# Kernel optimization log

Hardware: AMD Instinct MI355X
Metric: run time of the kernel (lower is better)

## Reference

```python
import jax, jax.numpy as jnp
import numpy as np

H, C, HID, L, NF, B = 4, 128, 128, 3, 5, 32  # heads, per-head dim, hidden, layers, node feats, graphs
LN_EPS = 1e-5


def setup_inputs() -> dict:
    key = jax.random.key(0)
    ks = jax.random.split(key, 12)
    N, E = 10000, 160000
    x = jax.random.normal(ks[0], (N, NF), dtype=jnp.float32)
    edge_index = jax.random.randint(ks[1], (2, E), 0, N, dtype=jnp.int64)
    batch = jnp.sort(jax.random.randint(ks[2], (N,), 0, B, dtype=jnp.int64))
    s = 0.1
    return {
        "x": x,
        "edge_index": edge_index,
        "batch": batch,
        "node_W": jax.random.normal(ks[3], (NF, HID), dtype=jnp.float32) * s,
        "node_b": jnp.zeros((HID,), dtype=jnp.float32),
        "Ws": jax.random.normal(ks[4], (L, HID, H * C), dtype=jnp.float32) * s,
        "att_srcs": jax.random.normal(ks[5], (L, H, C), dtype=jnp.float32) * s,
        "att_dsts": jax.random.normal(ks[6], (L, H, C), dtype=jnp.float32) * s,
        "biases": jnp.zeros((L, HID), dtype=jnp.float32),
        "ln_gs": jnp.ones((L, HID), dtype=jnp.float32),
        "ln_bs": jnp.zeros((L, HID), dtype=jnp.float32),
    }


def _layer_norm(x, g, b):
    mu = jnp.mean(x, axis=-1, keepdims=True)
    var = jnp.mean(jnp.square(x - mu), axis=-1, keepdims=True)
    return (x - mu) * jax.lax.rsqrt(var + LN_EPS) * g + b


def _gat_layer(x, W, att_src, att_dst, bias, src, dst, N):
    # x: [N, HID]; PyG GATConv, heads=H, concat=False (mean over heads)
    h = (x @ W).reshape(N, H, C)                       # [N,H,C]
    a_src = jnp.sum(h * att_src, axis=-1)              # [N,H]
    a_dst = jnp.sum(h * att_dst, axis=-1)              # [N,H]
    e = jax.nn.leaky_relu(a_src[src] + a_dst[dst], 0.2)  # [E,H]
    # edge-softmax over destination neighborhoods (numerically stable)
    m = jax.ops.segment_max(e, dst, num_segments=N)
    ex = jnp.exp(e - m[dst])
    denom = jax.ops.segment_sum(ex, dst, num_segments=N)
    alpha = ex / (denom[dst] + 1e-16)                  # [E,H]
    msg = h[src] * alpha[:, :, None]                   # [E,H,C]
    out = jax.ops.segment_sum(msg, dst, num_segments=N)  # [N,H,C]
    return out.mean(axis=1) + bias                     # concat=False -> head mean


def reference(x, edge_index, batch, node_W, node_b, Ws, att_srcs, att_dsts,
              biases, ln_gs, ln_bs):
    N = x.shape[0]
    loop = jnp.arange(N, dtype=edge_index.dtype)
    src = jnp.concatenate([edge_index[0], loop])       # PyG adds self-loops
    dst = jnp.concatenate([edge_index[1], loop])

    h = jax.nn.relu(x @ node_W + node_b)               # [N,HID]
    for l in range(L):
        h_new = _gat_layer(h, Ws[l], att_srcs[l], att_dsts[l], biases[l], src, dst, N)
        h_new = _layer_norm(h_new, ln_gs[l], ln_bs[l])
        h = jax.nn.relu(h_new) + h                     # residual; dropout is identity in eval

    # global mean pool over graphs
    sums = jax.ops.segment_sum(h, batch, num_segments=B)
    cnts = jax.ops.segment_sum(jnp.ones((N, 1), h.dtype), batch, num_segments=B)
    graph_emb = sums / jnp.maximum(cnts, 1.0)
    return h, graph_emb
```

## Files before the change

### kernel.cpp

```cpp
#include <hip/hip_runtime.h>
#include <math.h>

#define N_NODES 10000
#define N_EDGES 160000
#define E2 (N_EDGES + N_NODES)
#define HIDDEN 128
#define NHEAD 4
#define NB 32
#define LN_EPS 1e-5f

#define T_INPUT (N_NODES * HIDDEN)
#define T_HIST  (T_INPUT + N_EDGES)
#define T_CONV  (T_HIST + 3 * 512 * 128)
#define T_BOUND (T_CONV + N_NODES)
#define T_TOTAL T_BOUND

typedef __attribute__((ext_vector_type(8))) short bf16x8;
typedef __attribute__((ext_vector_type(4))) float f32x4;

__device__ __forceinline__ unsigned short f2bf(float f) {
    unsigned int u = __float_as_uint(f);
    u += 0x7fffu + ((u >> 16) & 1u);
    return (unsigned short)(u >> 16);
}
__device__ __forceinline__ float bf2f_lo(unsigned int u) { return __uint_as_float(u << 16); }
__device__ __forceinline__ float bf2f_hi(unsigned int u) { return __uint_as_float(u & 0xffff0000u); }

__global__ __launch_bounds__(256) void k_pre(const float* __restrict__ x,
                                             const float* __restrict__ W,
                                             const float* __restrict__ b,
                                             const int* __restrict__ ei,
                                             const int* __restrict__ batch,
                                             const float* __restrict__ Ws,
                                             float* __restrict__ h,
                                             unsigned short* __restrict__ hb,
                                             int* counts, int* gstart, int* gend,
                                             unsigned short* __restrict__ Btb) {
    int t = blockIdx.x * blockDim.x + threadIdx.x;
    if (t < T_INPUT) {
        int n = t >> 7, c = t & 127;
        float s = b[c];
        #pragma unroll
        for (int k = 0; k < 5; k++) s += x[n * 5 + k] * W[k * HIDDEN + c];
        float r = fmaxf(s, 0.f);
        h[t] = r;
        hb[t] = f2bf(r);
    } else if (t < T_HIST) {
        int e = t - T_INPUT;
        atomicAdd(&counts[ei[N_EDGES + e]], 1);
    } else if (t < T_CONV) {
        int i = t - T_HIST;
        int l = i >> 16, rem = i & 65535;
        int n = rem >> 7, k = rem & 127;
        Btb[i] = f2bf(Ws[l * 65536 + k * 512 + n]);
    } else if (t < T_BOUND) {
        int n = t - T_CONV;
        int bb = batch[n];
        if (n == 0 || batch[n - 1] != bb) gstart[bb] = n;
        if (n == N_NODES - 1 || batch[n + 1] != bb) gend[bb] = n + 1;
    }
}

__global__ void k_scan(const int* __restrict__ counts, int* rowptr, int* cursor) {
    __shared__ int sums[1024];
    int t = threadIdx.x;
    const int per = 10;
    int base = t * per;
    int loc[per];
    int s = 0;
    for (int i = 0; i < per; i++) {
        int idx = base + i;
        int v = (idx < N_NODES) ? counts[idx] + 1 : 0;
        loc[i] = s; s += v;
    }
    sums[t] = s;
    __syncthreads();
    for (int off = 1; off < 1024; off <<= 1) {
        int v = (t >= off) ? sums[t - off] : 0;
        __syncthreads();
        sums[t] += v;
        __syncthreads();
    }
    int prefix = (t > 0) ? sums[t - 1] : 0;
    for (int i = 0; i < per; i++) {
        int idx = base + i;
        if (idx < N_NODES) { int r = prefix + loc[i]; rowptr[idx] = r; cursor[idx] = r; }
    }
    if (t == 1023) rowptr[N_NODES] = sums[1023];
}

__global__ void k_scatter(const int* __restrict__ ei, int* cursor, int* csr_src) {
    int e = blockIdx.x * blockDim.x + threadIdx.x;
    if (e < N_EDGES) {
        int s = ei[e], d = ei[N_EDGES + e];
        int pos = atomicAdd(&cursor[d], 1);
        csr_src[pos] = s;
    } else if (e < E2) {
        int n = e - N_EDGES;
        int pos = atomicAdd(&cursor[n], 1);
        csr_src[pos] = n;
    }
}

__global__ __launch_bounds__(256) void k_gemm_att(const unsigned short* __restrict__ Ab,
                                                  const unsigned short* __restrict__ Bt,
                                                  const float* __restrict__ ws,
                                                  const float* __restrict__ wd,
                                                  unsigned short* __restrict__ Cb,
                                                  float* __restrict__ a_src,
                                                  float* __restrict__ a_dst) {
    int wave = threadIdx.x >> 6, lane = threadIdx.x & 63;
    int q = lane >> 4, u = lane & 15;
    int h = blockIdx.x;
    int rowgrp = wave & 1, colhalf = wave >> 1;
    int mbase = blockIdx.y * 32 + rowgrp * 16;
    int colbase = h * 128 + colhalf * 64;
    int arow = mbase + u;
    if (arow > N_NODES - 1) arow = N_NODES - 1;
    bf16x8 a[4];
    #pragma unroll
    for (int k0 = 0; k0 < 4; k0++)
        a[k0] = *(const bf16x8*)(Ab + (size_t)arow * 128 + k0 * 32 + q * 8);
    f32x4 acc[4];
    #pragma unroll
    for (int nb = 0; nb < 4; nb++) acc[nb] = (f32x4){0.f, 0.f, 0.f, 0.f};
    #pragma unroll
    for (int nb = 0; nb < 4; nb++) {
        const unsigned short* bp = Bt + (size_t)(colbase + nb * 16 + u) * 128 + q * 8;
        #pragma unroll
        for (int k0 = 0; k0 < 4; k0++) {
            bf16x8 bfr = *(const bf16x8*)(bp + k0 * 32);
            acc[nb] = __builtin_amdgcn_mfma_f32_16x16x32_bf16(a[k0], bfr, acc[nb], 0, 0, 0);
        }
    }
    #pragma unroll
    for (int nb = 0; nb < 4; nb++) {
        int col = colbase + nb * 16 + u;
        #pragma unroll
        for (int r = 0; r < 4; r++) {
            int row = mbase + q * 4 + r;
            if (row < N_NODES) Cb[(size_t)row * 512 + col] = f2bf(acc[nb][r]);
        }
    }
    float ps[4] = {}, pd[4] = {};
    #pragma unroll
    for (int nb = 0; nb < 4; nb++) {
        int cl = colhalf * 64 + nb * 16 + u;
        float wsv = ws[h * 128 + cl], wdv = wd[h * 128 + cl];
        #pragma unroll
        for (int r = 0; r < 4; r++) { ps[r] += acc[nb][r] * wsv; pd[r] += acc[nb][r] * wdv; }
    }
    #pragma unroll
    for (int d = 1; d < 16; d <<= 1) {
        #pragma unroll
        for (int r = 0; r < 4; r++) {
            ps[r] += __shfl_xor(ps[r], d);
            pd[r] += __shfl_xor(pd[r], d);
        }
    }
    __shared__ float ls[2][2][16], ldd[2][2][16];
    if (u == 0) {
        #pragma unroll
        for (int r = 0; r < 4; r++) {
            ls[rowgrp][colhalf][q * 4 + r] = ps[r];
            ldd[rowgrp][colhalf][q * 4 + r] = pd[r];
        }
    }
    __syncthreads();
    if (colhalf == 0 && lane < 16) {
        int row = mbase + lane;
        if (row < N_NODES) {
            a_src[row * 4 + h] = ls[rowgrp][0][lane] + ls[rowgrp][1][lane];
            a_dst[row * 4 + h] = ldd[rowgrp][0][lane] + ldd[rowgrp][1][lane];
        }
    }
}

__global__ __launch_bounds__(256) void k_agg(const uint4* __restrict__ hb4,
                                             const int* __restrict__ rowptr,
                                             const int* __restrict__ csr,
                                             const float* __restrict__ a_src,
                                             const float* __restrict__ a_dst,
                                             const float* __restrict__ bias,
                                             const float* __restrict__ lng,
                                             const float* __restrict__ lnb,
                                             float* __restrict__ h,
                                             unsigned short* __restrict__ hbn) {
    int wave = threadIdx.x >> 6;
    int lane = threadIdx.x & 63;
    int n = blockIdx.x * 4 + wave;
    if (n >= N_NODES) return;
    int hl = lane >> 4;
    int pos = lane & 15;
    int off = rowptr[n];
    int deg = rowptr[n + 1] - off;
    float adn = a_dst[n * 4 + hl];
    float m = -INFINITY, denom = 0.f;
    float o[8] = {};
    for (int base = 0; base < deg; base += 64) {
        int cnt = min(64, deg - base);
        int s = (lane < cnt) ? csr[off + base + lane] : 0;
        int si = __shfl(s, 0);
        uint4 u = hb4[(size_t)si * 64 + lane];
        float av = a_src[si * 4 + hl];
        for (int i = 0; i < cnt; i++) {
            int inext = (i + 1 < cnt) ? i + 1 : i;
            int sj = __shfl(s, inext);
            uint4 un = hb4[(size_t)sj * 64 + lane];
            float an = a_src[sj * 4 + hl];
            float t = av + adn;
            float e = t > 0.f ? t : 0.2f * t;
            float nm = fmaxf(m, e);
            float sc = __expf(m - nm);
            float p = __expf(e - nm);
            denom = denom * sc + p;
            o[0] = o[0] * sc + p * bf2f_lo(u.x);
            o[1] = o[1] * sc + p * bf2f_hi(u.x);
            o[2] = o[2] * sc + p * bf2f_lo(u.y);
            o[3] = o[3] * sc + p * bf2f_hi(u.y);
            o[4] = o[4] * sc + p * bf2f_lo(u.z);
            o[5] = o[5] * sc + p * bf2f_hi(u.z);
            o[6] = o[6] * sc + p * bf2f_lo(u.w);
            o[7] = o[7] * sc + p * bf2f_hi(u.w);
            m = nm;
            u = un; av = an;
        }
    }
    float inv = 1.f / (denom + 1e-16f);
    #pragma unroll
    for (int k = 0; k < 8; k++) o[k] *= inv;
    #pragma unroll
    for (int k = 0; k < 8; k++) {
        o[k] += __shfl_xor(o[k], 16);
        o[k] += __shfl_xor(o[k], 32);
    }
    float v[8], sv = 0.f, sq = 0.f;
    #pragma unroll
    for (int k = 0; k < 8; k++) {
        float b = bias[8 * pos + k];
        v[k] = 0.25f * o[k] + b;
        sv += v[k]; sq += v[k] * v[k];
    }
    #pragma unroll
    for (int d = 8; d > 0; d >>= 1) {
        sv += __shfl_xor(sv, d);
        sq += __shfl_xor(sq, d);
    }
    float mu = sv * (1.f / 128.f);
    float var = sq * (1.f / 128.f) - mu * mu;
    float rs = rsqrtf(var + LN_EPS);
    if (hl == 0) {
        float* hrow = h + (size_t)n * 128 + 8 * pos;
        float4 old0 = *(const float4*)(hrow);
        float4 old1 = *(const float4*)(hrow + 4);
        float r[8];
        #pragma unroll
        for (int k = 0; k < 8; k++) {
            float y = (v[k] - mu) * rs * lng[8 * pos + k] + lnb[8 * pos + k];
            r[k] = fmaxf(y, 0.f);
        }
        float w[8] = {r[0] + old0.x, r[1] + old0.y, r[2] + old0.z, r[3] + old0.w,
                      r[4] + old1.x, r[5] + old1.y, r[6] + old1.z, r[7] + old1.w};
        *(float4*)(hrow) = make_float4(w[0], w[1], w[2], w[3]);
        *(float4*)(hrow + 4) = make_float4(w[4], w[5], w[6], w[7]);
        ushort4 p0, p1;
        p0.x = f2bf(w[0]); p0.y = f2bf(w[1]); p0.z = f2bf(w[2]); p0.w = f2bf(w[3]);
        p1.x = f2bf(w[4]); p1.y = f2bf(w[5]); p1.z = f2bf(w[6]); p1.w = f2bf(w[7]);
        unsigned short* hbrow = hbn + (size_t)n * 128 + 8 * pos;
        *(ushort4*)(hbrow) = p0;
        *(ushort4*)(hbrow + 4) = p1;
    }
}

#define POOL_CHUNK 32
__global__ __launch_bounds__(128) void k_pool_sum(const float* __restrict__ h,
                                                  const int* __restrict__ batch,
                                                  const int* __restrict__ gstart,
                                                  const int* __restrict__ gend,
                                                  float* __restrict__ gout) {
    int n0 = blockIdx.x * POOL_CHUNK;
    int c = threadIdx.x;
    int nend = min(n0 + POOL_CHUNK, N_NODES);
    if (n0 >= N_NODES) return;
    int cur = batch[n0];
    float acc = 0.f;
    for (int n = n0; n < nend; n++) {
        int b = batch[n];
        if (b != cur) {
            float inv = 1.f / (float)max(gend[cur] - gstart[cur], 1);
            atomicAdd(&gout[cur * HIDDEN + c], acc * inv);
            acc = 0.f; cur = b;
        }
        acc += h[(size_t)n * HIDDEN + c];
    }
    float inv = 1.f / (float)max(gend[cur] - gstart[cur], 1);
    atomicAdd(&gout[cur * HIDDEN + c], acc * inv);
}

extern "C" void kernel_launch(void* const* d_in, const int* in_sizes, int n_in,
                              void* d_out, int out_size, void* d_ws, size_t ws_size,
                              hipStream_t stream) {
    const float* x      = (const float*)d_in[0];
    const int*   ei     = (const int*)d_in[1];
    const int*   batch  = (const int*)d_in[2];
    const float* node_W = (const float*)d_in[3];
    const float* node_b = (const float*)d_in[4];
    const float* Ws     = (const float*)d_in[5];
    const float* att_s  = (const float*)d_in[6];
    const float* att_d  = (const float*)d_in[7];
    const float* biases = (const float*)d_in[8];
    const float* ln_g   = (const float*)d_in[9];
    const float* ln_b   = (const float*)d_in[10];

    float* out = (float*)d_out;
    float* h = out;
    float* gout = out + (size_t)N_NODES * HIDDEN;

    char* w = (char*)d_ws;
    auto carve = [&](size_t bytes) {
        void* p = (void*)w;
        w += (bytes + 255) & ~(size_t)255;
        return p;
    };
    int* rowptr  = (int*)carve((N_NODES + 1) * sizeof(int));
    int* cursor  = (int*)carve(N_NODES * sizeof(int));
    int* counts  = (int*)carve(N_NODES * sizeof(int));
    int* csr     = (int*)carve((E2 + 16) * sizeof(int));
    int* gstart  = (int*)carve(NB * sizeof(int));
    int* gend    = (int*)carve(NB * sizeof(int));
    float* a_src = (float*)carve((size_t)N_NODES * NHEAD * sizeof(float));
    float* a_dst = (float*)carve((size_t)N_NODES * NHEAD * sizeof(float));
    unsigned short* hb  = (unsigned short*)carve((size_t)N_NODES * 512 * sizeof(unsigned short));
    unsigned short* hbx = (unsigned short*)carve((size_t)N_NODES * HIDDEN * sizeof(unsigned short));
    unsigned short* Btb = (unsigned short*)carve((size_t)3 * 512 * 128 * sizeof(unsigned short));

    hipMemsetAsync(counts, 0, N_NODES * sizeof(int), stream);
    hipMemsetAsync(gout, 0, NB * HIDDEN * sizeof(float), stream);

    k_pre<<<(T_TOTAL + 255) / 256, 256, 0, stream>>>(x, node_W, node_b, ei, batch, Ws,
                                                     h, hbx, counts, gstart, gend, Btb);
    k_scan<<<1, 1024, 0, stream>>>(counts, rowptr, cursor);
    k_scatter<<<(E2 + 255) / 256, 256, 0, stream>>>(ei, cursor, csr);

    for (int l = 0; l < 3; l++) {
        k_gemm_att<<<dim3(4, (N_NODES + 31) / 32), 256, 0, stream>>>(
            hbx, Btb + (size_t)l * 512 * 128,
            att_s + l * NHEAD * 128, att_d + l * NHEAD * 128,
            hb, a_src, a_dst);
        k_agg<<<(N_NODES + 3) / 4, 256, 0, stream>>>((const uint4*)hb, rowptr, csr,
                                           a_src, a_dst,
                                           biases + l * HIDDEN, ln_g + l * HIDDEN,
                                           ln_b + l * HIDDEN, h, hbx);
    }
    k_pool_sum<<<(N_NODES + POOL_CHUNK - 1) / POOL_CHUNK, 128, 0, stream>>>(
        h, batch, gstart, gend, gout);
}
```

Measured before the change: 268.6 us.

## Replace online softmax in aggregation with two-pass max then lane-parallel exp weights

The per-edge online softmax in the aggregation kernel, which rescaled accumulators and evaluated two exps per edge serially, is replaced by a first pass that computes per-head maxima across lanes with wave reductions. A second pass computes the exp weights for 64 edges at once, one edge per lane, and stages them in LDS. The inner gather loop then only does multiply-adds with the weights read from shared memory. This removes serial exp and rescale work from the critical loop. In exchange, the CSR indices and a_src are read twice for high-degree nodes, and extra shuffle reductions and LDS traffic are added.

```diff
diff --git a/kernel.cpp b/kernel.cpp
--- a/kernel.cpp
+++ b/kernel.cpp
@@ -186,6 +186,7 @@
                                              const float* __restrict__ lnb,
                                              float* __restrict__ h,
                                              unsigned short* __restrict__ hbn) {
+    __shared__ float lp[4][4][68];
     int wave = threadIdx.x >> 6;
     int lane = threadIdx.x & 63;
     int n = blockIdx.x * 4 + wave;
@@ -194,39 +195,86 @@
     int pos = lane & 15;
     int off = rowptr[n];
     int deg = rowptr[n + 1] - off;
-    float adn = a_dst[n * 4 + hl];
-    float m = -INFINITY, denom = 0.f;
-    float o[8] = {};
+    float4 ad4 = *(const float4*)(a_dst + (size_t)n * 4);
+
+    float m0 = -INFINITY, m1 = -INFINITY, m2 = -INFINITY, m3 = -INFINITY;
+    float e0 = 0.f, e1 = 0.f, e2 = 0.f, e3 = 0.f;
+    int s_first = 0;
     for (int base = 0; base < deg; base += 64) {
         int cnt = min(64, deg - base);
-        int s = (lane < cnt) ? csr[off + base + lane] : 0;
-        int si = __shfl(s, 0);
-        uint4 u = hb4[(size_t)si * 64 + lane];
-        float av = a_src[si * 4 + hl];
+        int s = csr[off + base + ((lane < cnt) ? lane : cnt - 1)];
+        float4 av = *(const float4*)(a_src + (size_t)s * 4);
+        float t0 = av.x + ad4.x; float f0 = t0 > 0.f ? t0 : 0.2f * t0;
+        float t1 = av.y + ad4.y; float f1 = t1 > 0.f ? t1 : 0.2f * t1;
+        float t2 = av.z + ad4.z; float f2 = t2 > 0.f ? t2 : 0.2f * t2;
+        float t3 = av.w + ad4.w; float f3 = t3 > 0.f ? t3 : 0.2f * t3;
+        if (base == 0) { e0 = f0; e1 = f1; e2 = f2; e3 = f3; s_first = s; }
+        if (lane < cnt) {
+            m0 = fmaxf(m0, f0); m1 = fmaxf(m1, f1);
+            m2 = fmaxf(m2, f2); m3 = fmaxf(m3, f3);
+        }
+    }
+    #pragma unroll
+    for (int d = 1; d < 64; d <<= 1) {
+        m0 = fmaxf(m0, __shfl_xor(m0, d));
+        m1 = fmaxf(m1, __shfl_xor(m1, d));
+        m2 = fmaxf(m2, __shfl_xor(m2, d));
+        m3 = fmaxf(m3, __shfl_xor(m3, d));
+    }
+
+    float d0 = 0.f, d1 = 0.f, d2 = 0.f, d3 = 0.f;
+    float o[8] = {};
+    const float* lph = &lp[wave][0][0] + hl * 68;
+    for (int base = 0; base < deg; base += 64) {
+        int cnt = min(64, deg - base);
+        int s; float f0, f1, f2, f3;
+        if (base == 0) {
+            s = s_first; f0 = e0; f1 = e1; f2 = e2; f3 = e3;
+        } else {
+            s = csr[off + base + ((lane < cnt) ? lane : cnt - 1)];
+            float4 av = *(const float4*)(a_src + (size_t)s * 4);
+            float t0 = av.x + ad4.x; f0 = t0 > 0.f ? t0 : 0.2f * t0;
+            float t1 = av.y + ad4.y; f1 = t1 > 0.f ? t1 : 0.2f * t1;
+            float t2 = av.z + ad4.z; f2 = t2 > 0.f ? t2 : 0.2f * t2;
+            float t3 = av.w + ad4.w; f3 = t3 > 0.f ? t3 : 0.2f * t3;
+        }
+        float p0 = __expf(f0 - m0), p1 = __expf(f1 - m1);
+        float p2 = __expf(f2 - m2), p3 = __expf(f3 - m3);
+        if (lane >= cnt) { p0 = 0.f; p1 = 0.f; p2 = 0.f; p3 = 0.f; }
+        d0 += p0; d1 += p1; d2 += p2; d3 += p3;
+        lp[wave][0][lane] = p0;
+        lp[wave][1][lane] = p1;
+        lp[wave][2][lane] = p2;
+        lp[wave][3][lane] = p3;
+        asm volatile("s_waitcnt lgkmcnt(0)" ::: "memory");
+        int s0b = __shfl(s, 0);
+        uint4 u = hb4[(size_t)s0b * 64 + lane];
+        float p = lph[0];
         for (int i = 0; i < cnt; i++) {
             int inext = (i + 1 < cnt) ? i + 1 : i;
             int sj = __shfl(s, inext);
             uint4 un = hb4[(size_t)sj * 64 + lane];
-            float an = a_src[sj * 4 + hl];
-            float t = av + adn;
-            float e = t > 0.f ? t : 0.2f * t;
-            float nm = fmaxf(m, e);
-            float sc = __expf(m - nm);
-            float p = __expf(e - nm);
-            denom = denom * sc + p;
-            o[0] = o[0] * sc + p * bf2f_lo(u.x);
-            o[1] = o[1] * sc + p * bf2f_hi(u.x);
-            o[2] = o[2] * sc + p * bf2f_lo(u.y);
-            o[3] = o[3] * sc + p * bf2f_hi(u.y);
-            o[4] = o[4] * sc + p * bf2f_lo(u.z);
-            o[5] = o[5] * sc + p * bf2f_hi(u.z);
-            o[6] = o[6] * sc + p * bf2f_lo(u.w);
-            o[7] = o[7] * sc + p * bf2f_hi(u.w);
-            m = nm;
-            u = un; av = an;
-        }
-    }
-    float inv = 1.f / (denom + 1e-16f);
+            float pn = lph[inext];
+            o[0] += p * bf2f_lo(u.x);
+            o[1] += p * bf2f_hi(u.x);
+            o[2] += p * bf2f_lo(u.y);
+            o[3] += p * bf2f_hi(u.y);
+            o[4] += p * bf2f_lo(u.z);
+            o[5] += p * bf2f_hi(u.z);
+            o[6] += p * bf2f_lo(u.w);
+            o[7] += p * bf2f_hi(u.w);
+            u = un; p = pn;
+        }
+    }
+    #pragma unroll
+    for (int d = 1; d < 64; d <<= 1) {
+        d0 += __shfl_xor(d0, d);
+        d1 += __shfl_xor(d1, d);
+        d2 += __shfl_xor(d2, d);
+        d3 += __shfl_xor(d3, d);
+    }
+    float den = (hl == 0) ? d0 : ((hl == 1) ? d1 : ((hl == 2) ? d2 : d3));
+    float inv = 1.f / (den + 1e-16f);
     #pragma unroll
     for (int k = 0; k < 8; k++) o[k] *= inv;
     #pragma unroll
```

Result: no change. 270.2 us (+0.6%).

## Fuse graph mean-pool into last aggregation layer and deepen gather prefetch

Applied to the files above, without the earlier changes.

Removes the separate pooling kernel by having the final-layer aggregation kernel atomically add each node's scaled output into the graph embedding, with the behaviour selected through a template flag. The neighbor-gather loop now prefetches two edges ahead instead of one to hide more of the memory latency. In exchange, the pooling step issues one atomic per node feature (1.28M atomics onto 32x128 addresses) instead of one per 32-node chunk, which can cause heavy contention, and the deeper prefetch raises register use.

```diff
diff --git a/kernel.cpp b/kernel.cpp
--- a/kernel.cpp
+++ b/kernel.cpp
@@ -176,6 +176,7 @@
     }
 }
 
+template <int DO_POOL>
 __global__ __launch_bounds__(256) void k_agg(const uint4* __restrict__ hb4,
                                              const int* __restrict__ rowptr,
                                              const int* __restrict__ csr,
@@ -185,7 +186,11 @@
                                              const float* __restrict__ lng,
                                              const float* __restrict__ lnb,
                                              float* __restrict__ h,
-                                             unsigned short* __restrict__ hbn) {
+                                             unsigned short* __restrict__ hbn,
+                                             const int* __restrict__ batch,
+                                             const int* __restrict__ gstart,
+                                             const int* __restrict__ gend,
+                                             float* __restrict__ gout) {
     int wave = threadIdx.x >> 6;
     int lane = threadIdx.x & 63;
     int n = blockIdx.x * 4 + wave;
@@ -200,30 +205,35 @@
     for (int base = 0; base < deg; base += 64) {
         int cnt = min(64, deg - base);
         int s = (lane < cnt) ? csr[off + base + lane] : 0;
-        int si = __shfl(s, 0);
-        uint4 u = hb4[(size_t)si * 64 + lane];
-        float av = a_src[si * 4 + hl];
+        int j1 = (1 < cnt) ? 1 : 0;
+        int s0 = __shfl(s, 0);
+        int s1 = __shfl(s, j1);
+        uint4 u0 = hb4[(size_t)s0 * 64 + lane];
+        float a0 = a_src[s0 * 4 + hl];
+        uint4 u1 = hb4[(size_t)s1 * 64 + lane];
+        float a1 = a_src[s1 * 4 + hl];
         for (int i = 0; i < cnt; i++) {
-            int inext = (i + 1 < cnt) ? i + 1 : i;
-            int sj = __shfl(s, inext);
-            uint4 un = hb4[(size_t)sj * 64 + lane];
-            float an = a_src[sj * 4 + hl];
-            float t = av + adn;
+            int j2 = (i + 2 < cnt) ? i + 2 : cnt - 1;
+            int s2 = __shfl(s, j2);
+            uint4 u2 = hb4[(size_t)s2 * 64 + lane];
+            float a2 = a_src[s2 * 4 + hl];
+            float t = a0 + adn;
             float e = t > 0.f ? t : 0.2f * t;
             float nm = fmaxf(m, e);
             float sc = __expf(m - nm);
             float p = __expf(e - nm);
             denom = denom * sc + p;
-            o[0] = o[0] * sc + p * bf2f_lo(u.x);
-            o[1] = o[1] * sc + p * bf2f_hi(u.x);
-            o[2] = o[2] * sc + p * bf2f_lo(u.y);
-            o[3] = o[3] * sc + p * bf2f_hi(u.y);
-            o[4] = o[4] * sc + p * bf2f_lo(u.z);
-            o[5] = o[5] * sc + p * bf2f_hi(u.z);
-            o[6] = o[6] * sc + p * bf2f_lo(u.w);
-            o[7] = o[7] * sc + p * bf2f_hi(u.w);
+            o[0] = o[0] * sc + p * bf2f_lo(u0.x);
+            o[1] = o[1] * sc + p * bf2f_hi(u0.x);
+            o[2] = o[2] * sc + p * bf2f_lo(u0.y);
+            o[3] = o[3] * sc + p * bf2f_hi(u0.y);
+            o[4] = o[4] * sc + p * bf2f_lo(u0.z);
+            o[5] = o[5] * sc + p * bf2f_hi(u0.z);
+            o[6] = o[6] * sc + p * bf2f_lo(u0.w);
+            o[7] = o[7] * sc + p * bf2f_hi(u0.w);
             m = nm;
-            u = un; av = an;
+            u0 = u1; a0 = a1;
+            u1 = u2; a1 = a2;
         }
     }
     float inv = 1.f / (denom + 1e-16f);
@@ -269,32 +279,14 @@
         unsigned short* hbrow = hbn + (size_t)n * 128 + 8 * pos;
         *(ushort4*)(hbrow) = p0;
         *(ushort4*)(hbrow + 4) = p1;
-    }
-}
-
-#define POOL_CHUNK 32
-__global__ __launch_bounds__(128) void k_pool_sum(const float* __restrict__ h,
-                                                  const int* __restrict__ batch,
-                                                  const int* __restrict__ gstart,
-                                                  const int* __restrict__ gend,
-                                                  float* __restrict__ gout) {
-    int n0 = blockIdx.x * POOL_CHUNK;
-    int c = threadIdx.x;
-    int nend = min(n0 + POOL_CHUNK, N_NODES);
-    if (n0 >= N_NODES) return;
-    int cur = batch[n0];
-    float acc = 0.f;
-    for (int n = n0; n < nend; n++) {
-        int b = batch[n];
-        if (b != cur) {
-            float inv = 1.f / (float)max(gend[cur] - gstart[cur], 1);
-            atomicAdd(&gout[cur * HIDDEN + c], acc * inv);
-            acc = 0.f; cur = b;
-        }
-        acc += h[(size_t)n * HIDDEN + c];
-    }
-    float inv = 1.f / (float)max(gend[cur] - gstart[cur], 1);
-    atomicAdd(&gout[cur * HIDDEN + c], acc * inv);
+        if (DO_POOL) {
+            int g = batch[n];
+            float ic = 1.f / (float)max(gend[g] - gstart[g], 1);
+            #pragma unroll
+            for (int k = 0; k < 8; k++)
+                atomicAdd(&gout[g * HIDDEN + 8 * pos + k], w[k] * ic);
+        }
+    }
 }
 
 extern "C" void kernel_launch(void* const* d_in, const int* in_sizes, int n_in,
@@ -347,11 +339,18 @@
             hbx, Btb + (size_t)l * 512 * 128,
             att_s + l * NHEAD * 128, att_d + l * NHEAD * 128,
             hb, a_src, a_dst);
-        k_agg<<<(N_NODES + 3) / 4, 256, 0, stream>>>((const uint4*)hb, rowptr, csr,
-                                           a_src, a_dst,
-                                           biases + l * HIDDEN, ln_g + l * HIDDEN,
-                                           ln_b + l * HIDDEN, h, hbx);
-    }
-    k_pool_sum<<<(N_NODES + POOL_CHUNK - 1) / POOL_CHUNK, 128, 0, stream>>>(
-        h, batch, gstart, gend, gout);
-}
+        if (l < 2) {
+            k_agg<0><<<(N_NODES + 3) / 4, 256, 0, stream>>>((const uint4*)hb, rowptr, csr,
+                                               a_src, a_dst,
+                                               biases + l * HIDDEN, ln_g + l * HIDDEN,
+                                               ln_b + l * HIDDEN, h, hbx,
+                                               batch, gstart, gend, gout);
+        } else {
+            k_agg<1><<<(N_NODES + 3) / 4, 256, 0, stream>>>((const uint4*)hb, rowptr, csr,
+                                               a_src, a_dst,
+                                               biases + l * HIDDEN, ln_g + l * HIDDEN,
+                                               ln_b + l * HIDDEN, h, hbx,
+                                               batch, gstart, gend, gout);
+        }
+    }
+}
```

New measurement: 375.2 us. 39.7% more time.

## Split edge aggregation across two waves, fuse CSR scatter into GEMM, per-graph pooling

Applied to the files above, without the earlier changes.

The aggregation kernel now gives each node two waves, each covering alternate 64-edge chunks, and merges their online-softmax states through shared memory. This halves the serial per-node edge loop and doubles the waves in flight. The CSR scatter is folded into the first layer's GEMM launch, and pooling becomes one block per graph with no atomics or memset, removing two launches. The fused scatter runs in the same kernel that needs no CSR, so ordering is preserved; the cost is extra shared-memory traffic and a block-wide barrier in aggregation.

```diff
diff --git a/kernel.cpp b/kernel.cpp
--- a/kernel.cpp
+++ b/kernel.cpp
@@ -89,26 +89,29 @@
     if (t == 1023) rowptr[N_NODES] = sums[1023];
 }
 
-__global__ void k_scatter(const int* __restrict__ ei, int* cursor, int* csr_src) {
-    int e = blockIdx.x * blockDim.x + threadIdx.x;
-    if (e < N_EDGES) {
-        int s = ei[e], d = ei[N_EDGES + e];
-        int pos = atomicAdd(&cursor[d], 1);
-        csr_src[pos] = s;
-    } else if (e < E2) {
-        int n = e - N_EDGES;
-        int pos = atomicAdd(&cursor[n], 1);
-        csr_src[pos] = n;
-    }
-}
-
+template <int SCATTER>
 __global__ __launch_bounds__(256) void k_gemm_att(const unsigned short* __restrict__ Ab,
                                                   const unsigned short* __restrict__ Bt,
                                                   const float* __restrict__ ws,
                                                   const float* __restrict__ wd,
                                                   unsigned short* __restrict__ Cb,
                                                   float* __restrict__ a_src,
-                                                  float* __restrict__ a_dst) {
+                                                  float* __restrict__ a_dst,
+                                                  const int* __restrict__ ei,
+                                                  int* __restrict__ cursor,
+                                                  int* __restrict__ csr_src) {
+    if (SCATTER) {
+        int e = (blockIdx.y * gridDim.x + blockIdx.x) * 256 + threadIdx.x;
+        if (e < N_EDGES) {
+            int s = ei[e], d = ei[N_EDGES + e];
+            int pos = atomicAdd(&cursor[d], 1);
+            csr_src[pos] = s;
+        } else if (e < E2) {
+            int n = e - N_EDGES;
+            int pos = atomicAdd(&cursor[n], 1);
+            csr_src[pos] = n;
+        }
+    }
     int wave = threadIdx.x >> 6, lane = threadIdx.x & 63;
     int q = lane >> 4, u = lane & 15;
     int h = blockIdx.x;
@@ -186,46 +189,65 @@
                                              const float* __restrict__ lnb,
                                              float* __restrict__ h,
                                              unsigned short* __restrict__ hbn) {
-    int wave = threadIdx.x >> 6;
+    __shared__ float sm[2][64][10];
+    int w = threadIdx.x >> 6;
     int lane = threadIdx.x & 63;
-    int n = blockIdx.x * 4 + wave;
-    if (n >= N_NODES) return;
+    int nb = w >> 1;
+    int half = w & 1;
+    int n = blockIdx.x * 2 + nb;
     int hl = lane >> 4;
     int pos = lane & 15;
     int off = rowptr[n];
     int deg = rowptr[n + 1] - off;
     float adn = a_dst[n * 4 + hl];
-    float m = -INFINITY, denom = 0.f;
+    float m = -INFINITY, d = 0.f;
     float o[8] = {};
-    for (int base = 0; base < deg; base += 64) {
+    for (int base = half * 64; base < deg; base += 128) {
         int cnt = min(64, deg - base);
         int s = (lane < cnt) ? csr[off + base + lane] : 0;
         int si = __shfl(s, 0);
-        uint4 u = hb4[(size_t)si * 64 + lane];
+        uint4 uu = hb4[(size_t)si * 64 + lane];
         float av = a_src[si * 4 + hl];
         for (int i = 0; i < cnt; i++) {
             int inext = (i + 1 < cnt) ? i + 1 : i;
             int sj = __shfl(s, inext);
             uint4 un = hb4[(size_t)sj * 64 + lane];
             float an = a_src[sj * 4 + hl];
-            float t = av + adn;
-            float e = t > 0.f ? t : 0.2f * t;
+            float tt = av + adn;
+            float e = tt > 0.f ? tt : 0.2f * tt;
             float nm = fmaxf(m, e);
             float sc = __expf(m - nm);
             float p = __expf(e - nm);
-            denom = denom * sc + p;
-            o[0] = o[0] * sc + p * bf2f_lo(u.x);
-            o[1] = o[1] * sc + p * bf2f_hi(u.x);
-            o[2] = o[2] * sc + p * bf2f_lo(u.y);
-            o[3] = o[3] * sc + p * bf2f_hi(u.y);
-            o[4] = o[4] * sc + p * bf2f_lo(u.z);
-            o[5] = o[5] * sc + p * bf2f_hi(u.z);
-            o[6] = o[6] * sc + p * bf2f_lo(u.w);
-            o[7] = o[7] * sc + p * bf2f_hi(u.w);
+            d = d * sc + p;
+            o[0] = o[0] * sc + p * bf2f_lo(uu.x);
+            o[1] = o[1] * sc + p * bf2f_hi(uu.x);
+            o[2] = o[2] * sc + p * bf2f_lo(uu.y);
+            o[3] = o[3] * sc + p * bf2f_hi(uu.y);
+            o[4] = o[4] * sc + p * bf2f_lo(uu.z);
+            o[5] = o[5] * sc + p * bf2f_hi(uu.z);
+            o[6] = o[6] * sc + p * bf2f_lo(uu.w);
+            o[7] = o[7] * sc + p * bf2f_hi(uu.w);
             m = nm;
-            u = un; av = an;
-        }
-    }
+            uu = un; av = an;
+        }
+    }
+    if (half == 1) {
+        sm[nb][lane][0] = m;
+        sm[nb][lane][1] = d;
+        #pragma unroll
+        for (int k = 0; k < 8; k++) sm[nb][lane][2 + k] = o[k];
+    }
+    __syncthreads();
+    if (half == 1) return;
+    float mB = sm[nb][lane][0];
+    float dB = sm[nb][lane][1];
+    float M = fmaxf(m, mB);
+    float sA = __expf(m - M);
+    float sB = (mB == -INFINITY) ? 0.f : __expf(mB - M);
+    float denom = d * sA + dB * sB;
+    #pragma unroll
+    for (int k = 0; k < 8; k++) o[k] = o[k] * sA + sm[nb][lane][2 + k] * sB;
+
     float inv = 1.f / (denom + 1e-16f);
     #pragma unroll
     for (int k = 0; k < 8; k++) o[k] *= inv;
@@ -242,9 +264,9 @@
         sv += v[k]; sq += v[k] * v[k];
     }
     #pragma unroll
-    for (int d = 8; d > 0; d >>= 1) {
-        sv += __shfl_xor(sv, d);
-        sq += __shfl_xor(sq, d);
+    for (int dd = 8; dd > 0; dd >>= 1) {
+        sv += __shfl_xor(sv, dd);
+        sq += __shfl_xor(sq, dd);
     }
     float mu = sv * (1.f / 128.f);
     float var = sq * (1.f / 128.f) - mu * mu;
@@ -259,42 +281,37 @@
             float y = (v[k] - mu) * rs * lng[8 * pos + k] + lnb[8 * pos + k];
             r[k] = fmaxf(y, 0.f);
         }
-        float w[8] = {r[0] + old0.x, r[1] + old0.y, r[2] + old0.z, r[3] + old0.w,
-                      r[4] + old1.x, r[5] + old1.y, r[6] + old1.z, r[7] + old1.w};
-        *(float4*)(hrow) = make_float4(w[0], w[1], w[2], w[3]);
-        *(float4*)(hrow + 4) = make_float4(w[4], w[5], w[6], w[7]);
+        float wv[8] = {r[0] + old0.x, r[1] + old0.y, r[2] + old0.z, r[3] + old0.w,
+                       r[4] + old1.x, r[5] + old1.y, r[6] + old1.z, r[7] + old1.w};
+        *(float4*)(hrow) = make_float4(wv[0], wv[1], wv[2], wv[3]);
+        *(float4*)(hrow + 4) = make_float4(wv[4], wv[5], wv[6], wv[7]);
         ushort4 p0, p1;
-        p0.x = f2bf(w[0]); p0.y = f2bf(w[1]); p0.z = f2bf(w[2]); p0.w = f2bf(w[3]);
-        p1.x = f2bf(w[4]); p1.y = f2bf(w[5]); p1.z = f2bf(w[6]); p1.w = f2bf(w[7]);
+        p0.x = f2bf(wv[0]); p0.y = f2bf(wv[1]); p0.z = f2bf(wv[2]); p0.w = f2bf(wv[3]);
+        p1.x = f2bf(wv[4]); p1.y = f2bf(wv[5]); p1.z = f2bf(wv[6]); p1.w = f2bf(wv[7]);
         unsigned short* hbrow = hbn + (size_t)n * 128 + 8 * pos;
         *(ushort4*)(hbrow) = p0;
         *(ushort4*)(hbrow + 4) = p1;
     }
 }
 
-#define POOL_CHUNK 32
-__global__ __launch_bounds__(128) void k_pool_sum(const float* __restrict__ h,
-                                                  const int* __restrict__ batch,
-                                                  const int* __restrict__ gstart,
-                                                  const int* __restrict__ gend,
-                                                  float* __restrict__ gout) {
-    int n0 = blockIdx.x * POOL_CHUNK;
-    int c = threadIdx.x;
-    int nend = min(n0 + POOL_CHUNK, N_NODES);
-    if (n0 >= N_NODES) return;
-    int cur = batch[n0];
+__global__ __launch_bounds__(512) void k_pool(const float* __restrict__ h,
+                                              const int* __restrict__ gstart,
+                                              const int* __restrict__ gend,
+                                              float* __restrict__ gout) {
+    __shared__ float sm[4][128];
+    int g = blockIdx.x;
+    int c = threadIdx.x & 127;
+    int r = threadIdx.x >> 7;
+    int s = gstart[g], e = gend[g];
     float acc = 0.f;
-    for (int n = n0; n < nend; n++) {
-        int b = batch[n];
-        if (b != cur) {
-            float inv = 1.f / (float)max(gend[cur] - gstart[cur], 1);
-            atomicAdd(&gout[cur * HIDDEN + c], acc * inv);
-            acc = 0.f; cur = b;
-        }
-        acc += h[(size_t)n * HIDDEN + c];
-    }
-    float inv = 1.f / (float)max(gend[cur] - gstart[cur], 1);
-    atomicAdd(&gout[cur * HIDDEN + c], acc * inv);
+    for (int n = s + r; n < e; n += 4)
+        acc += h[(size_t)n * 128 + c];
+    sm[r][c] = acc;
+    __syncthreads();
+    if (r == 0) {
+        float tot = sm[0][c] + sm[1][c] + sm[2][c] + sm[3][c];
+        gout[g * 128 + c] = tot / (float)max(e - s, 1);
+    }
 }
 
 extern "C" void kernel_launch(void* const* d_in, const int* in_sizes, int n_in,
@@ -335,23 +352,27 @@
     unsigned short* Btb = (unsigned short*)carve((size_t)3 * 512 * 128 * sizeof(unsigned short));
 
     hipMemsetAsync(counts, 0, N_NODES * sizeof(int), stream);
-    hipMemsetAsync(gout, 0, NB * HIDDEN * sizeof(float), stream);
 
     k_pre<<<(T_TOTAL + 255) / 256, 256, 0, stream>>>(x, node_W, node_b, ei, batch, Ws,
                                                      h, hbx, counts, gstart, gend, Btb);
     k_scan<<<1, 1024, 0, stream>>>(counts, rowptr, cursor);
-    k_scatter<<<(E2 + 255) / 256, 256, 0, stream>>>(ei, cursor, csr);
 
     for (int l = 0; l < 3; l++) {
-        k_gemm_att<<<dim3(4, (N_NODES + 31) / 32), 256, 0, stream>>>(
-            hbx, Btb + (size_t)l * 512 * 128,
-            att_s + l * NHEAD * 128, att_d + l * NHEAD * 128,
-            hb, a_src, a_dst);
-        k_agg<<<(N_NODES + 3) / 4, 256, 0, stream>>>((const uint4*)hb, rowptr, csr,
+        if (l == 0) {
+            k_gemm_att<1><<<dim3(4, (N_NODES + 31) / 32), 256, 0, stream>>>(
+                hbx, Btb + (size_t)l * 512 * 128,
+                att_s + l * NHEAD * 128, att_d + l * NHEAD * 128,
+                hb, a_src, a_dst, ei, cursor, csr);
+        } else {
+            k_gemm_att<0><<<dim3(4, (N_NODES + 31) / 32), 256, 0, stream>>>(
+                hbx, Btb + (size_t)l * 512 * 128,
+                att_s + l * NHEAD * 128, att_d + l * NHEAD * 128,
+                hb, a_src, a_dst, ei, cursor, csr);
+        }
+        k_agg<<<N_NODES / 2, 256, 0, stream>>>((const uint4*)hb, rowptr, csr,
                                            a_src, a_dst,
                                            biases + l * HIDDEN, ln_g + l * HIDDEN,
                                            ln_b + l * HIDDEN, h, hbx);
     }
-    k_pool_sum<<<(N_NODES + POOL_CHUNK - 1) / POOL_CHUNK, 128, 0, stream>>>(
-        h, batch, gstart, gend, gout);
-}
+    k_pool<<<NB, 512, 0, stream>>>(h, gstart, gend, gout);
+}
```

New measurement: 293.6 us. 1.09x slower.
